# Performance work log

Measured on AMD Instinct MI355X. Metric: run time of the kernel, lower is better.

Reference implementation:

```python
import jax, jax.numpy as jnp
import numpy as np

N_NODES = 50000
N_EDGES = 800000
D_IN = 64
D_OUT = 64


def setup_inputs() -> dict:
    key = jax.random.key(0)
    ks = jax.random.split(key, 7)
    features = jax.random.normal(ks[0], (N_NODES, D_IN), dtype=jnp.float32)
    # Linear(in,out,bias=False) weight: (out_features, in_features)
    W = jax.random.normal(ks[1], (D_OUT, D_IN), dtype=jnp.float32) / np.sqrt(D_IN)
    bias = jnp.zeros((D_OUT,), dtype=jnp.float32)
    skip_weight = jnp.ones((D_OUT,), dtype=jnp.float32)
    # sparse normalized adjacency as an edge list with scalar weights
    edge_src = jax.random.randint(ks[2], (N_EDGES,), 0, N_NODES, dtype=jnp.int32)
    edge_dst = jax.random.randint(ks[3], (N_EDGES,), 0, N_NODES, dtype=jnp.int32)
    edge_weight = jax.random.uniform(ks[4], (N_EDGES,), dtype=jnp.float32)
    return {
        "features": features,
        "W": W,
        "bias": bias,
        "skip_weight": skip_weight,
        "edge_weight": edge_weight,
        "edge_src": edge_src,
        "edge_dst": edge_dst,
    }


def reference(features, W, bias, skip_weight, edge_weight, edge_src, edge_dst):
    # Feature transform: x @ W^T  -> (n, out_features)
    h = jnp.einsum("nd,od->no", features, W)
    # Skip term: elementwise scale of transformed features
    skip = h * skip_weight
    # Sparse SpMM: aggregate weighted neighbor messages
    msgs = h[edge_src] * edge_weight[:, None]          # (E, out)
    agg = jax.ops.segment_sum(msgs, edge_dst, num_segments=N_NODES)  # (n, out)
    out = skip + agg + bias
    return jax.nn.selu(out)
```

## Files before the change

### kernel.cpp

```cpp
#include <hip/hip_runtime.h>
#include <math.h>

#define N_NODES 50000
#define N_EDGES 800000
#define D 64
#define NB2 782
#define BCAP2 2048
#define EPB 4096

__device__ __forceinline__ float selu_f(float x) {
    const float scale = 1.0507009873554805f;
    const float alpha = 1.6732632423543772f;
    return x > 0.0f ? scale * x : scale * alpha * expm1f(x);
}

__device__ __forceinline__ unsigned int f2bf(float x) {
    unsigned int u = __float_as_uint(x);
    u += 0x7FFFu + ((u >> 16) & 1u);
    return u >> 16;
}

__device__ __forceinline__ float bf2f(unsigned short b) {
    return __uint_as_float((unsigned int)b << 16);
}

__global__ __launch_bounds__(256) void gemm_kernel(const float* __restrict__ feat,
                                                   const float* __restrict__ W,
                                                   const float* __restrict__ bias,
                                                   const float* __restrict__ skipw,
                                                   unsigned short* __restrict__ hb,
                                                   float* __restrict__ pre,
                                                   int* __restrict__ gcursor) {
    __shared__ float Wt[D][68];
    __shared__ float Sf[64][68];
    const int tid = threadIdx.x;
    const int base = blockIdx.x * 64;

    if (blockIdx.x == 0) {
        for (int i = tid; i < NB2; i += 256) gcursor[i] = 0;
    }

    for (int i = tid; i < D * D; i += 256) {
        int o = i >> 6, d = i & 63;
        Wt[d][o] = W[i];
    }
    for (int i = tid; i < 64 * D; i += 256) {
        int r = i >> 6, c = i & 63;
        int row = base + r;
        Sf[r][c] = (row < N_NODES) ? feat[(size_t)row * D + c] : 0.0f;
    }
    __syncthreads();

    const int wv = tid >> 6;
    const int lane = tid & 63;
    const int r = wv * 16 + (lane >> 2);
    const int cg = lane & 3;
    const int row = base + r;
    if (row >= N_NODES) return;

    float4 a0 = {0, 0, 0, 0}, a1 = {0, 0, 0, 0}, a2 = {0, 0, 0, 0}, a3 = {0, 0, 0, 0};
    const int c0 = cg * 16;
#pragma unroll 4
    for (int k = 0; k < D; ++k) {
        const float f = Sf[r][k];
        const float4 w0 = *(const float4*)&Wt[k][c0 + 0];
        const float4 w1 = *(const float4*)&Wt[k][c0 + 4];
        const float4 w2 = *(const float4*)&Wt[k][c0 + 8];
        const float4 w3 = *(const float4*)&Wt[k][c0 + 12];
        a0.x += f * w0.x; a0.y += f * w0.y; a0.z += f * w0.z; a0.w += f * w0.w;
        a1.x += f * w1.x; a1.y += f * w1.y; a1.z += f * w1.z; a1.w += f * w1.w;
        a2.x += f * w2.x; a2.y += f * w2.y; a2.z += f * w2.z; a2.w += f * w2.w;
        a3.x += f * w3.x; a3.y += f * w3.y; a3.z += f * w3.z; a3.w += f * w3.w;
    }

    const size_t obase = (size_t)row * D + c0;

    uint4 p0, p1;
    p0.x = f2bf(a0.x) | (f2bf(a0.y) << 16);
    p0.y = f2bf(a0.z) | (f2bf(a0.w) << 16);
    p0.z = f2bf(a1.x) | (f2bf(a1.y) << 16);
    p0.w = f2bf(a1.z) | (f2bf(a1.w) << 16);
    p1.x = f2bf(a2.x) | (f2bf(a2.y) << 16);
    p1.y = f2bf(a2.z) | (f2bf(a2.w) << 16);
    p1.z = f2bf(a3.x) | (f2bf(a3.y) << 16);
    p1.w = f2bf(a3.z) | (f2bf(a3.w) << 16);
    ((uint4*)(hb + obase))[0] = p0;
    ((uint4*)(hb + obase))[1] = p1;

    const float4* sk4 = (const float4*)skipw;
    const float4* b4 = (const float4*)bias;
    float4* pr4 = (float4*)(pre + obase);
    const int g4 = cg * 4;
    float4 s, b, o;
    s = sk4[g4 + 0]; b = b4[g4 + 0];
    o.x = a0.x * s.x + b.x; o.y = a0.y * s.y + b.y; o.z = a0.z * s.z + b.z; o.w = a0.w * s.w + b.w;
    pr4[0] = o;
    s = sk4[g4 + 1]; b = b4[g4 + 1];
    o.x = a1.x * s.x + b.x; o.y = a1.y * s.y + b.y; o.z = a1.z * s.z + b.z; o.w = a1.w * s.w + b.w;
    pr4[1] = o;
    s = sk4[g4 + 2]; b = b4[g4 + 2];
    o.x = a2.x * s.x + b.x; o.y = a2.y * s.y + b.y; o.z = a2.z * s.z + b.z; o.w = a2.w * s.w + b.w;
    pr4[2] = o;
    s = sk4[g4 + 3]; b = b4[g4 + 3];
    o.x = a3.x * s.x + b.x; o.y = a3.y * s.y + b.y; o.z = a3.z * s.z + b.z; o.w = a3.w * s.w + b.w;
    pr4[3] = o;
}

__global__ __launch_bounds__(1024) void scatter_ms(const int* __restrict__ edst,
                                                   const int* __restrict__ esrc,
                                                   const float* __restrict__ ew,
                                                   int* __restrict__ gcursor,
                                                   int2* __restrict__ pay) {
    __shared__ int hist[NB2];
    __shared__ int lexcl[NB2];
    __shared__ int gbase[NB2];
    __shared__ int waveAgg[16];
    __shared__ int2 stage[EPB];

    const int tid = threadIdx.x;
    const int wid = tid >> 6;
    const int lane = tid & 63;
    const int e0 = blockIdx.x * EPB;
    const int cntb = min(EPB, N_EDGES - e0);

    for (int i = tid; i < NB2; i += 1024) hist[i] = 0;
    __syncthreads();

    int2 rec[4];
    int rb[4];
#pragma unroll
    for (int k = 0; k < 4; ++k) {
        const int idx = k * 1024 + tid;
        rb[k] = -1;
        if (idx < cntb) {
            const int e = e0 + idx;
            const int dst = edst[e];
            const int b = dst >> 6;
            rb[k] = b;
            rec[k] = make_int2((esrc[e] & 0xFFFF) | ((dst & 63) << 16) | (b << 22),
                               __float_as_int(ew[e]));
            atomicAdd(&hist[b], 1);
        }
    }
    __syncthreads();

    const int v = (tid < NB2) ? hist[tid] : 0;
    int incl = v;
#pragma unroll
    for (int off = 1; off < 64; off <<= 1) {
        const int t = __shfl_up(incl, off);
        if (lane >= off) incl += t;
    }
    if (lane == 63) waveAgg[wid] = incl;
    __syncthreads();
    if (wid == 0) {
        const int wv = (lane < 16) ? waveAgg[lane] : 0;
        int wincl = wv;
#pragma unroll
        for (int off = 1; off < 16; off <<= 1) {
            const int t = __shfl_up(wincl, off);
            if (lane >= off) wincl += t;
        }
        if (lane < 16) waveAgg[lane] = wincl - wv;
    }
    __syncthreads();
    if (tid < NB2) {
        const int excl = incl - v + waveAgg[wid];
        lexcl[tid] = excl;
        hist[tid] = excl;
        gbase[tid] = (v > 0) ? atomicAdd(&gcursor[tid], v) : 0;
    }
    __syncthreads();

#pragma unroll
    for (int k = 0; k < 4; ++k) {
        if (rb[k] >= 0) {
            const int p = atomicAdd(&hist[rb[k]], 1);
            stage[p] = rec[k];
        }
    }
    __syncthreads();

    for (int i = tid; i < cntb; i += 1024) {
        const int2 r = stage[i];
        const int b = ((unsigned int)r.x) >> 22;
        const int g = gbase[b] + (i - lexcl[b]);
        if (g < BCAP2) pay[(size_t)b * BCAP2 + g] = r;
    }
}

__global__ __launch_bounds__(512) void csr_sort(const int* __restrict__ gcursor,
                                                int2* __restrict__ pay,
                                                int2* __restrict__ nodeinfo) {
    __shared__ int2 stage[BCAP2];
    __shared__ int cntL[64], curL[64];

    const int b = blockIdx.x;
    const int tid = threadIdx.x;
    const int cnt = min(gcursor[b], BCAP2);
    int2* payb = pay + (size_t)b * BCAP2;

    if (tid < 64) cntL[tid] = 0;
    __syncthreads();

    for (int i = tid; i < cnt; i += 512) {
        const int2 r = payb[i];
        stage[i] = r;
        atomicAdd(&cntL[(r.x >> 16) & 63], 1);
    }
    __syncthreads();

    if (tid < 64) {
        const int v = cntL[tid];
        int incl = v;
#pragma unroll
        for (int off = 1; off < 64; off <<= 1) {
            const int t = __shfl_up(incl, off);
            if (tid >= off) incl += t;
        }
        const int excl = incl - v;
        curL[tid] = excl;
        const int node = (b << 6) + tid;
        if (node < N_NODES) nodeinfo[node] = make_int2(b * BCAP2 + excl, v);
    }
    __syncthreads();

    for (int i = tid; i < cnt; i += 512) {
        const int2 r = stage[i];
        const int p = atomicAdd(&curL[(r.x >> 16) & 63], 1);
        payb[p] = r;
    }
}

__global__ __launch_bounds__(256) void agg_epilogue_kernel(const unsigned short* __restrict__ hb,
                                                           const int2* __restrict__ nodeinfo,
                                                           const int2* __restrict__ sorted_sw,
                                                           float* __restrict__ out) {
    const int gtid = blockIdx.x * 256 + threadIdx.x;
    const int n = gtid >> 6;
    const int lane = gtid & 63;
    if (n >= N_NODES) return;

    const int2 info = nodeinfo[n];
    const int beg = info.x;
    const int deg = info.y;

    float a0 = 0.f, a1 = 0.f, a2 = 0.f, a3 = 0.f;
    for (int i = 0; i < deg; i += 64) {
        const int cnt = min(64, deg - i);
        int2 sw = make_int2(0, 0);
        if (lane < cnt) sw = sorted_sw[beg + i + lane];

        int j = 0;
        for (; j + 3 < cnt; j += 4) {
            const int s0 = __shfl(sw.x, j + 0) & 0xFFFF;
            const int s1 = __shfl(sw.x, j + 1) & 0xFFFF;
            const int s2 = __shfl(sw.x, j + 2) & 0xFFFF;
            const int s3 = __shfl(sw.x, j + 3) & 0xFFFF;
            const float w0 = __int_as_float(__shfl(sw.y, j + 0));
            const float w1 = __int_as_float(__shfl(sw.y, j + 1));
            const float w2 = __int_as_float(__shfl(sw.y, j + 2));
            const float w3 = __int_as_float(__shfl(sw.y, j + 3));
            const float g0 = bf2f(hb[(size_t)s0 * D + lane]);
            const float g1 = bf2f(hb[(size_t)s1 * D + lane]);
            const float g2 = bf2f(hb[(size_t)s2 * D + lane]);
            const float g3 = bf2f(hb[(size_t)s3 * D + lane]);
            a0 += g0 * w0;
            a1 += g1 * w1;
            a2 += g2 * w2;
            a3 += g3 * w3;
        }
        for (; j < cnt; ++j) {
            const int s = __shfl(sw.x, j) & 0xFFFF;
            const float w = __int_as_float(__shfl(sw.y, j));
            a0 += bf2f(hb[(size_t)s * D + lane]) * w;
        }
    }

    const size_t idx = (size_t)n * D + lane;
    out[idx] = selu_f(out[idx] + ((a0 + a1) + (a2 + a3)));
}

extern "C" void kernel_launch(void* const* d_in, const int* in_sizes, int n_in,
                              void* d_out, int out_size, void* d_ws, size_t ws_size,
                              hipStream_t stream) {
    const float* feat  = (const float*)d_in[0];
    const float* W     = (const float*)d_in[1];
    const float* bias  = (const float*)d_in[2];
    const float* skipw = (const float*)d_in[3];
    const float* ew    = (const float*)d_in[4];
    const int*   esrc  = (const int*)d_in[5];
    const int*   edst  = (const int*)d_in[6];
    float* out = (float*)d_out;

    int2*           pay      = (int2*)d_ws;
    unsigned short* hb       = (unsigned short*)(pay + (size_t)NB2 * BCAP2);
    int2*           nodeinfo = (int2*)(hb + (size_t)N_NODES * D);
    int*            gcursor  = (int*)(nodeinfo + N_NODES);

    gemm_kernel<<<(N_NODES + 63) / 64, 256, 0, stream>>>(feat, W, bias, skipw, hb, out, gcursor);

    scatter_ms<<<(N_EDGES + EPB - 1) / EPB, 1024, 0, stream>>>(edst, esrc, ew, gcursor, pay);

    csr_sort<<<NB2, 512, 0, stream>>>(gcursor, pay, nodeinfo);

    agg_epilogue_kernel<<<(N_NODES * 64 + 255) / 256, 256, 0, stream>>>(
        hb, nodeinfo, pay, out);
}
```

Baseline: 143.2 us.

## Gather two bf16 features per lane and compute skip term in epilogue

The aggregation kernel now splits each 64-lane wave into two halves. Each half handles alternate edges and loads 4 bytes (two bf16 features) per lane instead of 2, and the halves are combined with a cross-half shuffle. The GEMM no longer writes an fp32 skip+bias pre-activation to the output buffer. The epilogue instead recomputes the skip term from the bf16 h row, which removes a full fp32 write and read of the output. In exchange the skip term now uses bf16-rounded h, which slightly reduces precision, and half the lanes sit idle at the final store.

```diff
diff --git a/kernel.cpp b/kernel.cpp
--- a/kernel.cpp
+++ b/kernel.cpp
@@ -20,16 +20,13 @@
     return u >> 16;
 }
 
-__device__ __forceinline__ float bf2f(unsigned short b) {
-    return __uint_as_float((unsigned int)b << 16);
+__device__ __forceinline__ float bf2f(unsigned int b) {
+    return __uint_as_float(b << 16);
 }
 
 __global__ __launch_bounds__(256) void gemm_kernel(const float* __restrict__ feat,
                                                    const float* __restrict__ W,
-                                                   const float* __restrict__ bias,
-                                                   const float* __restrict__ skipw,
                                                    unsigned short* __restrict__ hb,
-                                                   float* __restrict__ pre,
                                                    int* __restrict__ gcursor) {
     __shared__ float Wt[D][68];
     __shared__ float Sf[64][68];
@@ -74,7 +71,6 @@
     }
 
     const size_t obase = (size_t)row * D + c0;
-
     uint4 p0, p1;
     p0.x = f2bf(a0.x) | (f2bf(a0.y) << 16);
     p0.y = f2bf(a0.z) | (f2bf(a0.w) << 16);
@@ -86,24 +82,6 @@
     p1.w = f2bf(a3.z) | (f2bf(a3.w) << 16);
     ((uint4*)(hb + obase))[0] = p0;
     ((uint4*)(hb + obase))[1] = p1;
-
-    const float4* sk4 = (const float4*)skipw;
-    const float4* b4 = (const float4*)bias;
-    float4* pr4 = (float4*)(pre + obase);
-    const int g4 = cg * 4;
-    float4 s, b, o;
-    s = sk4[g4 + 0]; b = b4[g4 + 0];
-    o.x = a0.x * s.x + b.x; o.y = a0.y * s.y + b.y; o.z = a0.z * s.z + b.z; o.w = a0.w * s.w + b.w;
-    pr4[0] = o;
-    s = sk4[g4 + 1]; b = b4[g4 + 1];
-    o.x = a1.x * s.x + b.x; o.y = a1.y * s.y + b.y; o.z = a1.z * s.z + b.z; o.w = a1.w * s.w + b.w;
-    pr4[1] = o;
-    s = sk4[g4 + 2]; b = b4[g4 + 2];
-    o.x = a2.x * s.x + b.x; o.y = a2.y * s.y + b.y; o.z = a2.z * s.z + b.z; o.w = a2.w * s.w + b.w;
-    pr4[2] = o;
-    s = sk4[g4 + 3]; b = b4[g4 + 3];
-    o.x = a3.x * s.x + b.x; o.y = a3.y * s.y + b.y; o.z = a3.z * s.z + b.z; o.w = a3.w * s.w + b.w;
-    pr4[3] = o;
 }
 
 __global__ __launch_bounds__(1024) void scatter_ms(const int* __restrict__ edst,
@@ -234,51 +212,78 @@
 
 __global__ __launch_bounds__(256) void agg_epilogue_kernel(const unsigned short* __restrict__ hb,
                                                            const int2* __restrict__ nodeinfo,
-                                                           const int2* __restrict__ sorted_sw,
+                                                           const int2* __restrict__ pay,
+                                                           const float* __restrict__ bias,
+                                                           const float* __restrict__ skipw,
                                                            float* __restrict__ out) {
     const int gtid = blockIdx.x * 256 + threadIdx.x;
     const int n = gtid >> 6;
     const int lane = gtid & 63;
     if (n >= N_NODES) return;
 
+    const int half = lane >> 5;
+    const int sl = lane & 31;
+
     const int2 info = nodeinfo[n];
     const int beg = info.x;
     const int deg = info.y;
 
-    float a0 = 0.f, a1 = 0.f, a2 = 0.f, a3 = 0.f;
+    float a0x = 0.f, a0y = 0.f, a1x = 0.f, a1y = 0.f;
+    float a2x = 0.f, a2y = 0.f, a3x = 0.f, a3y = 0.f;
+
     for (int i = 0; i < deg; i += 64) {
         const int cnt = min(64, deg - i);
         int2 sw = make_int2(0, 0);
-        if (lane < cnt) sw = sorted_sw[beg + i + lane];
+        if (lane < cnt) sw = pay[beg + i + lane];
 
         int j = 0;
-        for (; j + 3 < cnt; j += 4) {
-            const int s0 = __shfl(sw.x, j + 0) & 0xFFFF;
-            const int s1 = __shfl(sw.x, j + 1) & 0xFFFF;
-            const int s2 = __shfl(sw.x, j + 2) & 0xFFFF;
-            const int s3 = __shfl(sw.x, j + 3) & 0xFFFF;
-            const float w0 = __int_as_float(__shfl(sw.y, j + 0));
-            const float w1 = __int_as_float(__shfl(sw.y, j + 1));
-            const float w2 = __int_as_float(__shfl(sw.y, j + 2));
-            const float w3 = __int_as_float(__shfl(sw.y, j + 3));
-            const float g0 = bf2f(hb[(size_t)s0 * D + lane]);
-            const float g1 = bf2f(hb[(size_t)s1 * D + lane]);
-            const float g2 = bf2f(hb[(size_t)s2 * D + lane]);
-            const float g3 = bf2f(hb[(size_t)s3 * D + lane]);
-            a0 += g0 * w0;
-            a1 += g1 * w1;
-            a2 += g2 * w2;
-            a3 += g3 * w3;
-        }
-        for (; j < cnt; ++j) {
+        for (; j + 7 < cnt; j += 8) {
+            const int s0 = __shfl(sw.x, j + 0 + half) & 0xFFFF;
+            const int s1 = __shfl(sw.x, j + 2 + half) & 0xFFFF;
+            const int s2 = __shfl(sw.x, j + 4 + half) & 0xFFFF;
+            const int s3 = __shfl(sw.x, j + 6 + half) & 0xFFFF;
+            const float w0 = __int_as_float(__shfl(sw.y, j + 0 + half));
+            const float w1 = __int_as_float(__shfl(sw.y, j + 2 + half));
+            const float w2 = __int_as_float(__shfl(sw.y, j + 4 + half));
+            const float w3 = __int_as_float(__shfl(sw.y, j + 6 + half));
+            const unsigned int g0 = *(const unsigned int*)(hb + ((size_t)s0 << 6) + sl * 2);
+            const unsigned int g1 = *(const unsigned int*)(hb + ((size_t)s1 << 6) + sl * 2);
+            const unsigned int g2 = *(const unsigned int*)(hb + ((size_t)s2 << 6) + sl * 2);
+            const unsigned int g3 = *(const unsigned int*)(hb + ((size_t)s3 << 6) + sl * 2);
+            a0x += bf2f(g0 & 0xFFFF) * w0;  a0y += bf2f(g0 >> 16) * w0;
+            a1x += bf2f(g1 & 0xFFFF) * w1;  a1y += bf2f(g1 >> 16) * w1;
+            a2x += bf2f(g2 & 0xFFFF) * w2;  a2y += bf2f(g2 >> 16) * w2;
+            a3x += bf2f(g3 & 0xFFFF) * w3;  a3y += bf2f(g3 >> 16) * w3;
+        }
+        for (; j + 1 < cnt; j += 2) {
+            const int s = __shfl(sw.x, j + half) & 0xFFFF;
+            const float w = __int_as_float(__shfl(sw.y, j + half));
+            const unsigned int g = *(const unsigned int*)(hb + ((size_t)s << 6) + sl * 2);
+            a0x += bf2f(g & 0xFFFF) * w;  a0y += bf2f(g >> 16) * w;
+        }
+        if (j < cnt) {
             const int s = __shfl(sw.x, j) & 0xFFFF;
             const float w = __int_as_float(__shfl(sw.y, j));
-            a0 += bf2f(hb[(size_t)s * D + lane]) * w;
-        }
-    }
-
-    const size_t idx = (size_t)n * D + lane;
-    out[idx] = selu_f(out[idx] + ((a0 + a1) + (a2 + a3)));
+            const unsigned int g = *(const unsigned int*)(hb + ((size_t)s << 6) + sl * 2);
+            const float m = (half == 0) ? 1.0f : 0.0f;
+            a1x += bf2f(g & 0xFFFF) * w * m;  a1y += bf2f(g >> 16) * w * m;
+        }
+    }
+
+    float sx = (a0x + a1x) + (a2x + a3x);
+    float sy = (a0y + a1y) + (a2y + a3y);
+    sx += __shfl_xor(sx, 32);
+    sy += __shfl_xor(sy, 32);
+
+    const unsigned int hn = *(const unsigned int*)(hb + ((size_t)n << 6) + sl * 2);
+    const float2 kv = ((const float2*)skipw)[sl];
+    const float2 bv = ((const float2*)bias)[sl];
+    if (half == 0) {
+        float2 o;
+        o.x = selu_f(bf2f(hn & 0xFFFF) * kv.x + bv.x + sx);
+        o.y = selu_f(bf2f(hn >> 16) * kv.y + bv.y + sy);
+        ((float2*)(out + ((size_t)n << 6)))[sl] = o;
+    }
 }
 
 extern "C" void kernel_launch(void* const* d_in, const int* in_sizes, int n_in,
@@ -298,12 +303,12 @@
     int2*           nodeinfo = (int2*)(hb + (size_t)N_NODES * D);
     int*            gcursor  = (int*)(nodeinfo + N_NODES);
 
-    gemm_kernel<<<(N_NODES + 63) / 64, 256, 0, stream>>>(feat, W, bias, skipw, hb, out, gcursor);
+    gemm_kernel<<<(N_NODES + 63) / 64, 256, 0, stream>>>(feat, W, hb, gcursor);
 
     scatter_ms<<<(N_EDGES + EPB - 1) / EPB, 1024, 0, stream>>>(edst, esrc, ew, gcursor, pay);
 
     csr_sort<<<NB2, 512, 0, stream>>>(gcursor, pay, nodeinfo);
 
     agg_epilogue_kernel<<<(N_NODES * 64 + 255) / 256, 256, 0, stream>>>(
-        hb, nodeinfo, pay, out);
-}
+        hb, nodeinfo, pay, bias, skipw, out);
+}
```

After: 137.3 us. 1.04x faster.
